# Kernel optimization log

Hardware: AMD Instinct MI355X
Metric: run time of the kernel (lower is better)

## Reference

```python
import jax, jax.numpy as jnp
import numpy as np

DIM_MODEL = 1024
DIM_K = 1024
DIM_V = 1024


def setup_inputs() -> dict:
    key = jax.random.key(0)
    ks = jax.random.split(key, 7)
    B, S = 4, 2048
    scale = 1.0 / np.sqrt(DIM_MODEL)
    return {
        "x": jax.random.normal(ks[0], (B, S, DIM_MODEL), dtype=jnp.float32),
        # weights stored [in, out] (transpose of torch Linear.weight)
        "Wq": jax.random.normal(ks[1], (DIM_MODEL, DIM_K), dtype=jnp.float32) * scale,
        "Wk": jax.random.normal(ks[2], (DIM_MODEL, DIM_K), dtype=jnp.float32) * scale,
        "Wv": jax.random.normal(ks[3], (DIM_MODEL, DIM_V), dtype=jnp.float32) * scale,
        "Wo": jax.random.normal(ks[4], (DIM_V, DIM_MODEL), dtype=jnp.float32) * (1.0 / np.sqrt(DIM_V)),
        "ln2_gamma": jnp.ones((DIM_MODEL,), dtype=jnp.float32),
        "ln2_beta": jnp.zeros((DIM_MODEL,), dtype=jnp.float32),
    }


def _layernorm(x, gamma, beta, eps=1e-5):
    mu = jnp.mean(x, axis=-1, keepdims=True)
    var = jnp.var(x, axis=-1, keepdims=True)
    return (x - mu) * jax.lax.rsqrt(var + eps) * gamma + beta


def reference(x, Wq, Wk, Wv, Wo, ln2_gamma, ln2_beta):
    # single-head attention, x: [B,S,D]
    q = jnp.einsum("bsd,dk->bsk", x, Wq)
    k = jnp.einsum("bsd,dk->bsk", x, Wk)
    v = jnp.einsum("bsd,dv->bsv", x, Wv)
    scores = jnp.einsum("bqk,bsk->bqs", q, k) / jnp.sqrt(jnp.asarray(DIM_K, x.dtype))
    attn = jax.nn.softmax(scores, axis=-1)  # [B,S,S]
    ctx = jnp.einsum("bqs,bsv->bqv", attn, v)
    hidden = jnp.einsum("bqv,vd->bqd", ctx, Wo)
    hidden = _layernorm(hidden, ln2_gamma, ln2_beta)
    return hidden
```

## Files before the change

kernel.cpp:

```cpp
#include <hip/hip_runtime.h>
#include <hip/hip_bf16.h>
#include <stdint.h>

typedef __bf16 bf16;
typedef __attribute__((ext_vector_type(8))) __bf16 bf16x8;
typedef __attribute__((ext_vector_type(4))) __bf16 bf16x4;
typedef __attribute__((ext_vector_type(4))) float f32x4;

#define AS1 __attribute__((address_space(1)))
#define AS3 __attribute__((address_space(3)))

__device__ __forceinline__ void gl_lds16(const void* g, void* l) {
  __builtin_amdgcn_global_load_lds((const AS1 uint32_t*)g, (AS3 uint32_t*)l, 16, 0, 0);
}

template <int MODE>
__global__ __launch_bounds__(256) void gemm128(
    const bf16* __restrict__ Abase, const bf16* __restrict__ Bbase,
    bf16* __restrict__ Cbase, int K, int lda, int ldb, int ldc,
    long long sA, long long sB, long long sC, float alpha,
    float* __restrict__ lsum, bf16* __restrict__ Vt) {
  extern __shared__ char smem[];
  const int z = blockIdx.z;
  const bf16* A = Abase + (long long)z * sA;
  const bf16* B = Bbase + (long long)z * sB;
  bf16* C = Cbase + (long long)z * sC;
  const int m0 = blockIdx.y * 128, n0 = blockIdx.x * 128;
  const int t = threadIdx.x;
  const int lane = t & 63, wave = t >> 6;
  const int wm = (wave >> 1) * 64, wn = (wave & 1) * 64;
  const int quad = lane >> 4, r = lane & 15;

  const int srow = t >> 3;
  const int schunk = (t & 7) ^ (srow & 7);
  const bf16* ga = A + (long long)(m0 + srow) * lda + schunk * 8;
  const bf16* gb = B + (long long)(n0 + srow) * ldb + schunk * 8;
  char* la = smem + t * 16;
  char* lb = smem + 16384 + t * 16;

  f32x4 acc[4][4] = {};

  for (int k0 = 0; k0 < K; k0 += 64) {
    __syncthreads();
#pragma unroll
    for (int rd = 0; rd < 4; rd++) {
      gl_lds16(ga + (long long)(32 * rd) * lda, la + rd * 4096);
      gl_lds16(gb + (long long)(32 * rd) * ldb, lb + rd * 4096);
    }
    ga += 64;
    gb += 64;
    __syncthreads();

#pragma unroll
    for (int kk = 0; kk < 2; kk++) {
      bf16x8 af[4], bfr[4];
      const int csa = ((kk * 4 + quad) ^ (r & 7)) * 16;
      const char* pa = smem + (wm + r) * 128 + csa;
      const char* pb = smem + 16384 + (wn + r) * 128 + csa;
#pragma unroll
      for (int i = 0; i < 4; i++) af[i] = *(const bf16x8*)(pa + i * 2048);
#pragma unroll
      for (int j = 0; j < 4; j++) bfr[j] = *(const bf16x8*)(pb + j * 2048);
#pragma unroll
      for (int i = 0; i < 4; i++)
#pragma unroll
        for (int j = 0; j < 4; j++)
          acc[i][j] = __builtin_amdgcn_mfma_f32_16x16x32_bf16(af[i], bfr[j],
                                                              acc[i][j], 0, 0, 0);
    }
  }

  if constexpr (MODE == 3) {
    if (blockIdx.x >= 16) {
      bf16* T = (bf16*)smem;
      __syncthreads();
#pragma unroll
      for (int i = 0; i < 4; i++)
#pragma unroll
        for (int j = 0; j < 4; j++)
#pragma unroll
          for (int rg = 0; rg < 4; rg++) {
            const int m = wm + i * 16 + quad * 4 + rg;
            const int n = wn + j * 16 + r;
            T[n * 136 + m] = (bf16)acc[i][j][rg];
          }
      __syncthreads();
      const int v0 = n0 - 2048;
      const int zz = m0 >> 11;
      const int s0l = m0 & 2047;
      bf16* Vtb = Vt + (long long)zz * 1024 * 2048;
      const int c = t & 15;
#pragma unroll
      for (int p = 0; p < 8; p++) {
        const int n = p * 16 + (t >> 4);
        bf16x8 val = *(const bf16x8*)(T + n * 136 + c * 8);
        *(bf16x8*)(Vtb + (long long)(v0 + n) * 2048 + s0l + c * 8) = val;
      }
      return;
    }
  }

#pragma unroll
  for (int i = 0; i < 4; i++) {
    const int row0 = m0 + wm + i * 16 + quad * 4;
    float rsum[4] = {0.f, 0.f, 0.f, 0.f};
    float inv[4];
    if constexpr (MODE == 2) {
#pragma unroll
      for (int rg = 0; rg < 4; rg++)
        inv[rg] = 1.f / lsum[(long long)z * 2048 + row0 + rg];
    }
#pragma unroll
    for (int j = 0; j < 4; j++) {
      const int col = n0 + wn + j * 16 + r;
#pragma unroll
      for (int rg = 0; rg < 4; rg++) {
        float v = acc[i][j][rg] * alpha;
        if constexpr (MODE == 1) {
          bf16 eb = (bf16)__expf(v);
          C[(long long)(row0 + rg) * ldc + col] = eb;
          rsum[rg] += (float)eb;
        } else if constexpr (MODE == 2) {
          C[(long long)(row0 + rg) * ldc + col] = (bf16)(v * inv[rg]);
        } else {
          C[(long long)(row0 + rg) * ldc + col] = (bf16)v;
        }
      }
    }
    if constexpr (MODE == 1) {
#pragma unroll
      for (int rg = 0; rg < 4; rg++) {
#pragma unroll
        for (int off = 8; off >= 1; off >>= 1)
          rsum[rg] += __shfl_xor(rsum[rg], off);
        if (r == 0)
          atomicAdd(&lsum[(long long)z * 2048 + row0 + rg], rsum[rg]);
      }
    }
  }
}

template <int MODE>
__global__ __launch_bounds__(256) void gemm64(
    const bf16* __restrict__ Abase, const bf16* __restrict__ Bbase,
    bf16* __restrict__ Cbase, int K, int lda, int ldb, int ldc,
    long long sA, long long sB, long long sC, float alpha,
    float* __restrict__ lsum) {
  extern __shared__ char smem[];
  const int z = blockIdx.z;
  const bf16* A = Abase + (long long)z * sA;
  const bf16* B = Bbase + (long long)z * sB;
  bf16* C = Cbase + (long long)z * sC;
  const int m0 = blockIdx.y * 64, n0 = blockIdx.x * 128;
  const int t = threadIdx.x;
  const int lane = t & 63, wave = t >> 6;
  const int wm = (wave >> 1) * 32, wn = (wave & 1) * 64;
  const int quad = lane >> 4, r = lane & 15;

  const int srow = t >> 3;
  const int schunk = (t & 7) ^ (srow & 7);
  const bf16* ga = A + (long long)(m0 + srow) * lda + schunk * 8;
  const bf16* gb = B + (long long)(n0 + srow) * ldb + schunk * 8;
  char* la = smem + t * 16;
  char* lb = smem + 8192 + t * 16;

  f32x4 acc[2][4] = {};

  for (int k0 = 0; k0 < K; k0 += 64) {
    __syncthreads();
#pragma unroll
    for (int rd = 0; rd < 2; rd++)
      gl_lds16(ga + (long long)(32 * rd) * lda, la + rd * 4096);
#pragma unroll
    for (int rd = 0; rd < 4; rd++)
      gl_lds16(gb + (long long)(32 * rd) * ldb, lb + rd * 4096);
    ga += 64;
    gb += 64;
    __syncthreads();

#pragma unroll
    for (int kk = 0; kk < 2; kk++) {
      bf16x8 af[2], bfr[4];
      const int csa = ((kk * 4 + quad) ^ (r & 7)) * 16;
      const char* pa = smem + (wm + r) * 128 + csa;
      const char* pb = smem + 8192 + (wn + r) * 128 + csa;
#pragma unroll
      for (int i = 0; i < 2; i++) af[i] = *(const bf16x8*)(pa + i * 2048);
#pragma unroll
      for (int j = 0; j < 4; j++) bfr[j] = *(const bf16x8*)(pb + j * 2048);
#pragma unroll
      for (int i = 0; i < 2; i++)
#pragma unroll
        for (int j = 0; j < 4; j++)
          acc[i][j] = __builtin_amdgcn_mfma_f32_16x16x32_bf16(af[i], bfr[j],
                                                              acc[i][j], 0, 0, 0);
    }
  }

#pragma unroll
  for (int i = 0; i < 2; i++) {
    const int row0 = m0 + wm + i * 16 + quad * 4;
    float inv[4];
    if constexpr (MODE == 2) {
#pragma unroll
      for (int rg = 0; rg < 4; rg++)
        inv[rg] = 1.f / lsum[(long long)z * 2048 + row0 + rg];
    }
#pragma unroll
    for (int j = 0; j < 4; j++) {
      const int col = n0 + wn + j * 16 + r;
#pragma unroll
      for (int rg = 0; rg < 4; rg++) {
        float v = acc[i][j][rg] * alpha;
        if constexpr (MODE == 2) v *= inv[rg];
        C[(long long)(row0 + rg) * ldc + col] = (bf16)v;
      }
    }
  }
}

__global__ __launch_bounds__(256) void prep(
    const float* __restrict__ x, const float* __restrict__ Wq,
    const float* __restrict__ Wk, const float* __restrict__ Wv,
    const float* __restrict__ Wo, bf16* __restrict__ Xb,
    bf16* __restrict__ Wcat, bf16* __restrict__ Wot,
    float* __restrict__ lsum) {
  __shared__ float tile[32][33];
  const int bx = blockIdx.x;
  const int t = threadIdx.x;
  if (bx < 4096) {
    if (bx < 32) lsum[bx * 256 + t] = 0.f;
    long long i = (long long)bx * 256 + t;
    const float4* p = (const float4*)x;
    float4 a = p[i * 2], b = p[i * 2 + 1];
    bf16x8 o;
    o[0] = (bf16)a.x; o[1] = (bf16)a.y; o[2] = (bf16)a.z; o[3] = (bf16)a.w;
    o[4] = (bf16)b.x; o[5] = (bf16)b.y; o[6] = (bf16)b.z; o[7] = (bf16)b.w;
    ((bf16x8*)Xb)[i] = o;
  } else {
    int idx = bx - 4096;
    const int zw = idx >> 10;
    idx &= 1023;
    const int tiy = idx >> 5, tix = idx & 31;
    const float* W = (zw == 0) ? Wq : (zw == 1) ? Wk : (zw == 2) ? Wv : Wo;
    bf16* dst = (zw < 3) ? (Wcat + (long long)zw * 1024 * 1024) : Wot;
    const int bx0 = tix * 32, by0 = tiy * 32;
    const int ttx = t & 31, tty = t >> 5;
#pragma unroll
    for (int i = 0; i < 32; i += 8)
      tile[tty + i][ttx] = W[(long long)(by0 + tty + i) * 1024 + bx0 + ttx];
    __syncthreads();
#pragma unroll
    for (int i = 0; i < 32; i += 8)
      dst[(long long)(bx0 + tty + i) * 1024 + by0 + ttx] = (bf16)tile[ttx][tty + i];
  }
}

__global__ __launch_bounds__(256) void layernorm_rows(
    const bf16* __restrict__ H, const float* __restrict__ gamma,
    const float* __restrict__ beta, float* __restrict__ O) {
  const long long row = blockIdx.x;
  const bf16* h = H + row * 1024;
  float* o = O + row * 1024;
  const int t = threadIdx.x;
  const int lane = t & 63, wave = t >> 6;
  bf16x4 hv = ((const bf16x4*)h)[t];
  float v[4] = {(float)hv[0], (float)hv[1], (float)hv[2], (float)hv[3]};
  float s = v[0] + v[1] + v[2] + v[3];
  float ss = v[0] * v[0] + v[1] * v[1] + v[2] * v[2] + v[3] * v[3];
#pragma unroll
  for (int off = 32; off >= 1; off >>= 1) {
    s += __shfl_xor(s, off);
    ss += __shfl_xor(ss, off);
  }
  __shared__ float rs[4], rss[4];
  if (lane == 0) {
    rs[wave] = s;
    rss[wave] = ss;
  }
  __syncthreads();
  s = rs[0] + rs[1] + rs[2] + rs[3];
  ss = rss[0] + rss[1] + rss[2] + rss[3];
  const float mean = s * (1.f / 1024.f);
  const float var = ss * (1.f / 1024.f) - mean * mean;
  const float rstd = rsqrtf(var + 1e-5f);
  float4 g = ((const float4*)gamma)[t];
  float4 bb = ((const float4*)beta)[t];
  float4 rr;
  rr.x = (v[0] - mean) * rstd * g.x + bb.x;
  rr.y = (v[1] - mean) * rstd * g.y + bb.y;
  rr.z = (v[2] - mean) * rstd * g.z + bb.z;
  rr.w = (v[3] - mean) * rstd * g.w + bb.w;
  ((float4*)o)[t] = rr;
}

extern "C" void kernel_launch(void* const* d_in, const int* in_sizes, int n_in,
                              void* d_out, int out_size, void* d_ws,
                              size_t ws_size, hipStream_t stream) {
  const float* x = (const float*)d_in[0];
  const float* Wq = (const float*)d_in[1];
  const float* Wk = (const float*)d_in[2];
  const float* Wv = (const float*)d_in[3];
  const float* Wo = (const float*)d_in[4];
  const float* gamma = (const float*)d_in[5];
  const float* beta = (const float*)d_in[6];
  float* out = (float*)d_out;

  char* ws = (char*)d_ws;
  const size_t MB = 1024ull * 1024ull;
  bf16* Xb = (bf16*)(ws + 0);
  bf16* Wcat = (bf16*)(ws + 16 * MB);
  bf16* Wot = (bf16*)(ws + 22 * MB);
  bf16* QKV = (bf16*)(ws + 24 * MB);
  bf16* Vt = (bf16*)(ws + 72 * MB);
  bf16* expS = (bf16*)(ws + 88 * MB);
  float* lsum = (float*)(ws + 120 * MB);
  bf16* ctx = (bf16*)(ws + 121 * MB);
  bf16* Hd = (bf16*)(ws + 137 * MB);

  const long long bQKV = 2048LL * 3072;

  prep<<<8192, 256, 0, stream>>>(x, Wq, Wk, Wv, Wo, Xb, Wcat, Wot, lsum);

  gemm128<3><<<dim3(24, 64, 1), 256, 34816, stream>>>(
      Xb, Wcat, QKV, 1024, 1024, 1024, 3072, 0, 0, 0, 1.f, nullptr, Vt);

  gemm128<1><<<dim3(16, 16, 4), 256, 32768, stream>>>(
      QKV, QKV + 1024, expS, 1024, 3072, 3072, 2048, bQKV, bQKV,
      2048 * 2048LL, 0.03125f, lsum, nullptr);

  gemm64<2><<<dim3(8, 32, 4), 256, 24576, stream>>>(
      expS, Vt, ctx, 2048, 2048, 2048, 1024, 2048 * 2048LL, 1024 * 2048LL,
      2048 * 1024LL, 1.f, lsum);

  gemm64<0><<<dim3(8, 128, 1), 256, 24576, stream>>>(
      ctx, Wot, Hd, 1024, 1024, 1024, 1024, 0, 0, 0, 1.f, nullptr);

  layernorm_rows<<<8192, 256, 0, stream>>>(Hd, gamma, beta, out);
}
```

Before: 301.9 us.

## Reassociate attention output as P·(V·Wo) and split QKV into separate buffers

Computes V·Wo first as (Wo^T·V^T), giving a transposed VWo per batch, then multiplies the unnormalized exp-scores by VWo. This removes the separate ctx×Wo GEMM and the Vt transpose epilogue in the QKV projection, which now writes Q, K and V into separate contiguous buffers. The two smaller 64-row GEMM kernels are replaced with the 128x128 tile kernel. FLOP count stays about the same, since V·Wo costs as much as ctx·Wo. The change alters rounding order through an extra bf16 intermediate.

```diff
diff --git a/kernel.cpp b/kernel.cpp
--- a/kernel.cpp
+++ b/kernel.cpp
@@ -19,7 +19,7 @@
     const bf16* __restrict__ Abase, const bf16* __restrict__ Bbase,
     bf16* __restrict__ Cbase, int K, int lda, int ldb, int ldc,
     long long sA, long long sB, long long sC, float alpha,
-    float* __restrict__ lsum, bf16* __restrict__ Vt) {
+    float* __restrict__ lsum, bf16* __restrict__ C2, bf16* __restrict__ C3) {
   extern __shared__ char smem[];
   const int z = blockIdx.z;
   const bf16* A = Abase + (long long)z * sA;
@@ -70,34 +70,28 @@
     }
   }
 
-  if constexpr (MODE == 3) {
-    if (blockIdx.x >= 16) {
-      bf16* T = (bf16*)smem;
-      __syncthreads();
-#pragma unroll
-      for (int i = 0; i < 4; i++)
-#pragma unroll
-        for (int j = 0; j < 4; j++)
-#pragma unroll
-          for (int rg = 0; rg < 4; rg++) {
-            const int m = wm + i * 16 + quad * 4 + rg;
-            const int n = wn + j * 16 + r;
-            T[n * 136 + m] = (bf16)acc[i][j][rg];
-          }
-      __syncthreads();
-      const int v0 = n0 - 2048;
-      const int zz = m0 >> 11;
-      const int s0l = m0 & 2047;
-      bf16* Vtb = Vt + (long long)zz * 1024 * 2048;
-      const int c = t & 15;
-#pragma unroll
-      for (int p = 0; p < 8; p++) {
-        const int n = p * 16 + (t >> 4);
-        bf16x8 val = *(const bf16x8*)(T + n * 136 + c * 8);
-        *(bf16x8*)(Vtb + (long long)(v0 + n) * 2048 + s0l + c * 8) = val;
+  if constexpr (MODE == 4) {
+    bf16* dst;
+    int c0;
+    if (n0 < 1024) {
+      dst = Cbase; c0 = n0;
+    } else if (n0 < 2048) {
+      dst = C2; c0 = n0 - 1024;
+    } else {
+      dst = C3; c0 = n0 - 2048;
+    }
+#pragma unroll
+    for (int i = 0; i < 4; i++) {
+      const int row0 = m0 + wm + i * 16 + quad * 4;
+#pragma unroll
+      for (int j = 0; j < 4; j++) {
+        const int col = c0 + wn + j * 16 + r;
+#pragma unroll
+        for (int rg = 0; rg < 4; rg++)
+          dst[(long long)(row0 + rg) * 1024 + col] = (bf16)acc[i][j][rg];
       }
-      return;
-    }
+    }
+    return;
   }
 
 #pragma unroll
@@ -135,85 +129,6 @@
           rsum[rg] += __shfl_xor(rsum[rg], off);
         if (r == 0)
           atomicAdd(&lsum[(long long)z * 2048 + row0 + rg], rsum[rg]);
-      }
-    }
-  }
-}
-
-template <int MODE>
-__global__ __launch_bounds__(256) void gemm64(
-    const bf16* __restrict__ Abase, const bf16* __restrict__ Bbase,
-    bf16* __restrict__ Cbase, int K, int lda, int ldb, int ldc,
-    long long sA, long long sB, long long sC, float alpha,
-    float* __restrict__ lsum) {
-  extern __shared__ char smem[];
-  const int z = blockIdx.z;
-  const bf16* A = Abase + (long long)z * sA;
-  const bf16* B = Bbase + (long long)z * sB;
-  bf16* C = Cbase + (long long)z * sC;
-  const int m0 = blockIdx.y * 64, n0 = blockIdx.x * 128;
-  const int t = threadIdx.x;
-  const int lane = t & 63, wave = t >> 6;
-  const int wm = (wave >> 1) * 32, wn = (wave & 1) * 64;
-  const int quad = lane >> 4, r = lane & 15;
-
-  const int srow = t >> 3;
-  const int schunk = (t & 7) ^ (srow & 7);
-  const bf16* ga = A + (long long)(m0 + srow) * lda + schunk * 8;
-  const bf16* gb = B + (long long)(n0 + srow) * ldb + schunk * 8;
-  char* la = smem + t * 16;
-  char* lb = smem + 8192 + t * 16;
-
-  f32x4 acc[2][4] = {};
-
-  for (int k0 = 0; k0 < K; k0 += 64) {
-    __syncthreads();
-#pragma unroll
-    for (int rd = 0; rd < 2; rd++)
-      gl_lds16(ga + (long long)(32 * rd) * lda, la + rd * 4096);
-#pragma unroll
-    for (int rd = 0; rd < 4; rd++)
-      gl_lds16(gb + (long long)(32 * rd) * ldb, lb + rd * 4096);
-    ga += 64;
-    gb += 64;
-    __syncthreads();
-
-#pragma unroll
-    for (int kk = 0; kk < 2; kk++) {
-      bf16x8 af[2], bfr[4];
-      const int csa = ((kk * 4 + quad) ^ (r & 7)) * 16;
-      const char* pa = smem + (wm + r) * 128 + csa;
-      const char* pb = smem + 8192 + (wn + r) * 128 + csa;
-#pragma unroll
-      for (int i = 0; i < 2; i++) af[i] = *(const bf16x8*)(pa + i * 2048);
-#pragma unroll
-      for (int j = 0; j < 4; j++) bfr[j] = *(const bf16x8*)(pb + j * 2048);
-#pragma unroll
-      for (int i = 0; i < 2; i++)
-#pragma unroll
-        for (int j = 0; j < 4; j++)
-          acc[i][j] = __builtin_amdgcn_mfma_f32_16x16x32_bf16(af[i], bfr[j],
-                                                              acc[i][j], 0, 0, 0);
-    }
-  }
-
-#pragma unroll
-  for (int i = 0; i < 2; i++) {
-    const int row0 = m0 + wm + i * 16 + quad * 4;
-    float inv[4];
-    if constexpr (MODE == 2) {
-#pragma unroll
-      for (int rg = 0; rg < 4; rg++)
-        inv[rg] = 1.f / lsum[(long long)z * 2048 + row0 + rg];
-    }
-#pragma unroll
-    for (int j = 0; j < 4; j++) {
-      const int col = n0 + wn + j * 16 + r;
-#pragma unroll
-      for (int rg = 0; rg < 4; rg++) {
-        float v = acc[i][j][rg] * alpha;
-        if constexpr (MODE == 2) v *= inv[rg];
-        C[(long long)(row0 + rg) * ldc + col] = (bf16)v;
       }
     }
   }
@@ -311,30 +226,30 @@
   bf16* Xb = (bf16*)(ws + 0);
   bf16* Wcat = (bf16*)(ws + 16 * MB);
   bf16* Wot = (bf16*)(ws + 22 * MB);
-  bf16* QKV = (bf16*)(ws + 24 * MB);
-  bf16* Vt = (bf16*)(ws + 72 * MB);
-  bf16* expS = (bf16*)(ws + 88 * MB);
-  float* lsum = (float*)(ws + 120 * MB);
-  bf16* ctx = (bf16*)(ws + 121 * MB);
-  bf16* Hd = (bf16*)(ws + 137 * MB);
-
-  const long long bQKV = 2048LL * 3072;
+  bf16* Qd = (bf16*)(ws + 24 * MB);
+  bf16* Kd = (bf16*)(ws + 40 * MB);
+  bf16* Vd = (bf16*)(ws + 56 * MB);
+  bf16* expS = (bf16*)(ws + 72 * MB);
+  float* lsum = (float*)(ws + 104 * MB);
+  bf16* VWo = (bf16*)(ws + 105 * MB);
+  bf16* Hd = (bf16*)(ws + 121 * MB);
 
   prep<<<8192, 256, 0, stream>>>(x, Wq, Wk, Wv, Wo, Xb, Wcat, Wot, lsum);
 
-  gemm128<3><<<dim3(24, 64, 1), 256, 34816, stream>>>(
-      Xb, Wcat, QKV, 1024, 1024, 1024, 3072, 0, 0, 0, 1.f, nullptr, Vt);
+  gemm128<4><<<dim3(24, 64, 1), 256, 32768, stream>>>(
+      Xb, Wcat, Qd, 1024, 1024, 1024, 1024, 0, 0, 0, 1.f, nullptr, Kd, Vd);
 
   gemm128<1><<<dim3(16, 16, 4), 256, 32768, stream>>>(
-      QKV, QKV + 1024, expS, 1024, 3072, 3072, 2048, bQKV, bQKV,
-      2048 * 2048LL, 0.03125f, lsum, nullptr);
-
-  gemm64<2><<<dim3(8, 32, 4), 256, 24576, stream>>>(
-      expS, Vt, ctx, 2048, 2048, 2048, 1024, 2048 * 2048LL, 1024 * 2048LL,
-      2048 * 1024LL, 1.f, lsum);
-
-  gemm64<0><<<dim3(8, 128, 1), 256, 24576, stream>>>(
-      ctx, Wot, Hd, 1024, 1024, 1024, 1024, 0, 0, 0, 1.f, nullptr);
+      Qd, Kd, expS, 1024, 1024, 1024, 2048, 2048 * 1024LL, 2048 * 1024LL,
+      2048 * 2048LL, 0.03125f, lsum, nullptr, nullptr);
+
+  gemm128<0><<<dim3(16, 8, 4), 256, 32768, stream>>>(
+      Wot, Vd, VWo, 1024, 1024, 1024, 2048, 0, 2048 * 1024LL, 1024 * 2048LL,
+      1.f, nullptr, nullptr, nullptr);
+
+  gemm128<2><<<dim3(8, 16, 4), 256, 32768, stream>>>(
+      expS, VWo, Hd, 2048, 2048, 2048, 1024, 2048 * 2048LL, 1024 * 2048LL,
+      2048 * 1024LL, 1.f, lsum, nullptr, nullptr);
 
   layernorm_rows<<<8192, 256, 0, stream>>>(Hd, gamma, beta, out);
 }
```

Result: faster. 287.1 us (-4.9%).
